# Kernel tuning notes

Hardware: AMD Instinct MI355X
Metric: run time of the kernel (lower is better)

## Reference

```python
import jax, jax.numpy as jnp
import numpy as np
from jax import lax

DN = ('NCHW', 'OIHW', 'NCHW')

def setup_inputs() -> dict:
    key = jax.random.key(0)
    ks = jax.random.split(key, 7)
    s = 0.05  # keep activations tame through 32 chained blocks
    return {
        'x':  jax.random.normal(ks[0], (16, 256, 64, 64), dtype=jnp.float32),
        'w1': jax.random.normal(ks[1], (32, 4, 256, 1, 1), dtype=jnp.float32) * s,
        'b1': jax.random.normal(ks[2], (32, 4), dtype=jnp.float32) * s,
        'w2': jax.random.normal(ks[3], (32, 4, 4, 3, 3), dtype=jnp.float32) * s,
        'b2': jax.random.normal(ks[4], (32, 4), dtype=jnp.float32) * s,
        'w3': jax.random.normal(ks[5], (32, 256, 4, 1, 1), dtype=jnp.float32) * s,
        'b3': jax.random.normal(ks[6], (32, 256), dtype=jnp.float32) * s,
    }

def _block(x, w1, c1, w2, c2, w3, c3):
    # 1x1 reduce -> relu -> 3x3 same -> relu -> 1x1 expand -> relu
    h = jax.nn.relu(lax.conv_general_dilated(x, w1, (1, 1), 'VALID', dimension_numbers=DN)
                    + c1[None, :, None, None])
    h = jax.nn.relu(lax.conv_general_dilated(h, w2, (1, 1), 'SAME', dimension_numbers=DN)
                    + c2[None, :, None, None])
    h = jax.nn.relu(lax.conv_general_dilated(h, w3, (1, 1), 'VALID', dimension_numbers=DN)
                    + c3[None, :, None, None])
    return h

def reference(x, w1, b1, w2, b2, w3, b3):
    def step(carry, ws):
        xc, acc = carry
        xc = _block(xc, *ws)
        return (xc, acc + xc), None
    init = (x, jnp.zeros_like(x))
    (_, acc), _ = lax.scan(step, init, (w1, b1, w2, b2, w3, b3))
    return acc  # sum of all 32 block outputs, [16,256,64,64]
```

## Files before the change

### kernel.cpp

```cpp
#include <hip/hip_runtime.h>


#define NN 16
#define HH 64
#define WW 64
#define CIN 256
#define CB 4
#define NBLK 32
#define PXT 32

__device__ __forceinline__ int pxs(int px) { return px ^ ((px >> 3) & 7); }

__global__ __launch_bounds__(256) void phaseA(
    const float* __restrict__ x, const float* __restrict__ w1,
    const float* __restrict__ b1, float* __restrict__ h1out) {
  __shared__ float4 w1s[CIN];
  __shared__ float4 part[4][WW];
  int tid = threadIdx.x;
  for (int i = tid; i < CIN * CB; i += 256) {
    int o = i >> 8, c = i & 255;
    ((float*)&w1s[c])[o] = w1[i];
  }
  __syncthreads();
  int y = blockIdx.x, n = blockIdx.y;
  int chunk = tid >> 6, px = tid & 63;
  int cbase = chunk * 64;
  const float* xp = x + ((n * CIN + cbase) * HH + y) * WW + px;
  float s0 = 0.f, s1 = 0.f, s2 = 0.f, s3 = 0.f;
#pragma unroll 8
  for (int i = 0; i < 64; ++i) {
    float xv = xp[i * HH * WW];
    float4 wv = w1s[cbase + i];
    s0 = fmaf(xv, wv.x, s0);
    s1 = fmaf(xv, wv.y, s1);
    s2 = fmaf(xv, wv.z, s2);
    s3 = fmaf(xv, wv.w, s3);
  }
  part[chunk][px] = make_float4(s0, s1, s2, s3);
  __syncthreads();
  int px2 = tid >> 2, o = tid & 3;
  float v = ((float*)&part[0][px2])[o] + ((float*)&part[1][px2])[o] +
            ((float*)&part[2][px2])[o] + ((float*)&part[3][px2])[o];
  v += b1[o];
  h1out[((n * HH + y) * WW + px2) * CB + o] = fmaxf(v, 0.f);
}

__global__ __launch_bounds__(256) void phaseB(
    const float* __restrict__ h1in, float* __restrict__ h1out,
    float* __restrict__ h2out,
    const float* __restrict__ w2, const float* __restrict__ b2,
    const float* __restrict__ w3, const float* __restrict__ b3,
    const float* __restrict__ w1n, const float* __restrict__ b1n,
    int compute_next) {
  __shared__ float4 wpk[CIN][2];
  __shared__ float4 b3p[64];
  __shared__ __align__(16) float uni[8192];
  float4* h2pv = (float4*)uni;
  float4* combv = (float4*)uni;
  float4 (*h1t)[18] = (float4(*)[18])uni;

  int tid = threadIdx.x;
  int tx = blockIdx.x, ty = blockIdx.y, n = blockIdx.z;
  int x0 = tx * 16, y0 = ty * 16;

  {
    int c = tid;
    wpk[c][0] = *(const float4*)&w3[c * 4];
    float4 wt;
    wt.x = w1n[c];
    wt.y = w1n[256 + c];
    wt.z = w1n[512 + c];
    wt.w = w1n[768 + c];
    wpk[c][1] = wt;
    if (tid < 64) b3p[tid] = *(const float4*)&b3[tid * 4];
  }
  for (int t = tid; t < 324; t += 256) {
    int cy = t / 18, cx = t % 18;
    int gy = y0 + cy - 1, gx = x0 + cx - 1;
    float4 v = make_float4(0.f, 0.f, 0.f, 0.f);
    if (gy >= 0 && gy < HH && gx >= 0 && gx < WW)
      v = *(const float4*)&h1in[((n * HH + gy) * WW + gx) * CB];
    h1t[cy][cx] = v;
  }
  __syncthreads();

  int lx = tid & 15, ly = tid >> 4;

  float4 hacc = make_float4(b2[0], b2[1], b2[2], b2[3]);
#pragma unroll
  for (int p = 0; p < 9; ++p) {
    int dy = p / 3, dx = p % 3;
    float4 hv = h1t[ly + dy][lx + dx];
#pragma unroll
    for (int i = 0; i < 4; ++i) {
      float hvi = (i == 0) ? hv.x : (i == 1) ? hv.y : (i == 2) ? hv.z : hv.w;
      hacc.x = fmaf(hvi, w2[(0 * 4 + i) * 9 + p], hacc.x);
      hacc.y = fmaf(hvi, w2[(1 * 4 + i) * 9 + p], hacc.y);
      hacc.z = fmaf(hvi, w2[(2 * 4 + i) * 9 + p], hacc.z);
      hacc.w = fmaf(hvi, w2[(3 * 4 + i) * 9 + p], hacc.w);
    }
  }
  float4 h2 = make_float4(fmaxf(hacc.x, 0.f), fmaxf(hacc.y, 0.f),
                          fmaxf(hacc.z, 0.f), fmaxf(hacc.w, 0.f));

  int gy = y0 + ly, gx = x0 + lx;
  int pxg = (n * HH + gy) * WW + gx;
  *(float4*)&h2out[pxg * CB] = h2;

  __syncthreads();
  h2pv[pxs(tid)] = h2;
  __syncthreads();

  int pg = tid & 31, q = tid >> 5;
  float4 h2r[8];
#pragma unroll
  for (int j = 0; j < 8; ++j) h2r[j] = h2pv[pxs(pg * 8 + j)];

  float4 tp[8];
#pragma unroll
  for (int j = 0; j < 8; ++j) tp[j] = make_float4(0.f, 0.f, 0.f, 0.f);

  int cbase = q * 32;
  for (int i4 = 0; i4 < 8; ++i4) {
    float4 bv = b3p[q * 8 + i4];
#pragma unroll
    for (int s = 0; s < 4; ++s) {
      int c = cbase + i4 * 4 + s;
      float b = (s == 0) ? bv.x : (s == 1) ? bv.y : (s == 2) ? bv.z : bv.w;
      float4 w3v = wpk[c][0];
      float4 wnv = wpk[c][1];
#pragma unroll
      for (int j = 0; j < 8; ++j) {
        float u = fmaf(h2r[j].x, w3v.x, b);
        u = fmaf(h2r[j].y, w3v.y, u);
        u = fmaf(h2r[j].z, w3v.z, u);
        u = fmaf(h2r[j].w, w3v.w, u);
        float v = fmaxf(u, 0.f);
        tp[j].x = fmaf(v, wnv.x, tp[j].x);
        tp[j].y = fmaf(v, wnv.y, tp[j].y);
        tp[j].z = fmaf(v, wnv.z, tp[j].z);
        tp[j].w = fmaf(v, wnv.w, tp[j].w);
      }
    }
  }

  __syncthreads();
#pragma unroll
  for (int j = 0; j < 8; ++j)
    combv[q * 256 + pxs(pg * 8 + j)] = tp[j];
  __syncthreads();

  if (compute_next) {
    float4 t = combv[0 * 256 + pxs(tid)];
#pragma unroll
    for (int qq = 1; qq < 8; ++qq) {
      float4 pv = combv[qq * 256 + pxs(tid)];
      t.x += pv.x; t.y += pv.y; t.z += pv.z; t.w += pv.w;
    }
    float4 r = make_float4(fmaxf(t.x + b1n[0], 0.f), fmaxf(t.y + b1n[1], 0.f),
                           fmaxf(t.z + b1n[2], 0.f), fmaxf(t.w + b1n[3], 0.f));
    *(float4*)&h1out[pxg * CB] = r;
  }
}

__global__ __launch_bounds__(256, 4) void phaseC(
    const float* __restrict__ h2buf, const float* __restrict__ w3g,
    const float* __restrict__ b3g, float* __restrict__ out) {
  __shared__ float4 h2s[2][PXT];
  __shared__ float tr[CIN][PXT + 1];
  int tid = threadIdx.x;
  int p0 = blockIdx.x * PXT;
  int n = blockIdx.y;
  float acc[PXT];
#pragma unroll
  for (int i = 0; i < PXT; ++i) acc[i] = 0.f;

  if (tid < PXT)
    h2s[0][tid] = *(const float4*)&h2buf[((0 * NN + n) * 4096 + p0 + tid) * 4];
  __syncthreads();

  for (int k = 0; k < NBLK; ++k) {
    float4 wv = *(const float4*)&w3g[(k * 256 + tid) * 4];
    float bv = b3g[k * 256 + tid];
    if (k + 1 < NBLK && tid < PXT)
      h2s[(k + 1) & 1][tid] =
          *(const float4*)&h2buf[(((k + 1) * NN + n) * 4096 + p0 + tid) * 4];
    const float4* hb = h2s[k & 1];
#pragma unroll
    for (int i = 0; i < PXT; ++i) {
      float4 h = hb[i];
      float u = fmaf(h.w, wv.w,
                fmaf(h.z, wv.z, fmaf(h.y, wv.y, fmaf(h.x, wv.x, bv))));
      acc[i] += fmaxf(u, 0.f);
    }
    __syncthreads();
  }

#pragma unroll
  for (int i = 0; i < PXT; ++i) tr[tid][i] = acc[i];
  __syncthreads();
  int xi = tid & 31, cb = tid >> 5;
#pragma unroll
  for (int j = 0; j < 32; ++j) {
    int c = cb + j * 8;
    out[(n * CIN + c) * (HH * WW) + p0 + xi] = tr[c][xi];
  }
}

extern "C" void kernel_launch(void* const* d_in, const int* in_sizes, int n_in,
                              void* d_out, int out_size, void* d_ws, size_t ws_size,
                              hipStream_t stream) {
  const float* x  = (const float*)d_in[0];
  const float* w1 = (const float*)d_in[1];
  const float* b1 = (const float*)d_in[2];
  const float* w2 = (const float*)d_in[3];
  const float* b2 = (const float*)d_in[4];
  const float* w3 = (const float*)d_in[5];
  const float* b3 = (const float*)d_in[6];
  float* out = (float*)d_out;
  float* ws = (float*)d_ws;

  const int STATE = NN * HH * WW * CB;
  float* h1a = ws;
  float* h1b = ws + STATE;
  float* h2  = ws + 2 * STATE;

  phaseA<<<dim3(HH, NN), 256, 0, stream>>>(x, w1, b1, h1a);
  for (int k = 0; k < NBLK; ++k) {
    const float* hin = (k & 1) ? h1b : h1a;
    float* hout = (k & 1) ? h1a : h1b;
    int kn = (k < NBLK - 1) ? k + 1 : NBLK - 1;
    phaseB<<<dim3(4, 4, NN), 256, 0, stream>>>(
        hin, hout, h2 + k * STATE,
        w2 + k * 144, b2 + k * CB, w3 + k * 1024, b3 + k * 256,
        w1 + kn * 1024, b1 + kn * CB, (k < NBLK - 1) ? 1 : 0);
  }
  phaseC<<<dim3((HH * WW) / PXT, NN), 256, 0, stream>>>(h2, w3, b3, out);
}
```

Before: 515.3 us.

## Halve phaseB tile height to double grid and split channels across 16 groups

phaseB now processes 16x8 pixel tiles instead of 16x16, launching 512 blocks per block-step instead of 256 so more of the GPU's compute units are occupied during the 32 serial launches. The 3x3 conv uses only half the threads, and the fused expand/next-reduce work is split into 16 channel groups of 16 instead of 8 groups of 32, with a 16-way reduction in shared memory. Launch bounds request 2 blocks per SM. In exchange there is more halo overhead, idle threads during the 3x3 stage and a larger shared-memory reduction.

```diff
diff --git a/kernel.cpp b/kernel.cpp
--- a/kernel.cpp
+++ b/kernel.cpp
@@ -45,7 +45,7 @@
   h1out[((n * HH + y) * WW + px2) * CB + o] = fmaxf(v, 0.f);
 }
 
-__global__ __launch_bounds__(256) void phaseB(
+__global__ __launch_bounds__(256, 2) void phaseB(
     const float* __restrict__ h1in, float* __restrict__ h1out,
     float* __restrict__ h2out,
     const float* __restrict__ w2, const float* __restrict__ b2,
@@ -54,14 +54,14 @@
     int compute_next) {
   __shared__ float4 wpk[CIN][2];
   __shared__ float4 b3p[64];
-  __shared__ __align__(16) float uni[8192];
-  float4* h2pv = (float4*)uni;
-  float4* combv = (float4*)uni;
+  __shared__ float4 h2sb[128];
+  __shared__ __align__(16) float4 uni[2048];
   float4 (*h1t)[18] = (float4(*)[18])uni;
+  float4* comb = (float4*)uni;
 
   int tid = threadIdx.x;
   int tx = blockIdx.x, ty = blockIdx.y, n = blockIdx.z;
-  int x0 = tx * 16, y0 = ty * 16;
+  int x0 = tx * 16, y0 = ty * 8;
 
   {
     int c = tid;
@@ -74,8 +74,8 @@
     wpk[c][1] = wt;
     if (tid < 64) b3p[tid] = *(const float4*)&b3[tid * 4];
   }
-  for (int t = tid; t < 324; t += 256) {
-    int cy = t / 18, cx = t % 18;
+  if (tid < 180) {
+    int cy = tid / 18, cx = tid % 18;
     int gy = y0 + cy - 1, gx = x0 + cx - 1;
     float4 v = make_float4(0.f, 0.f, 0.f, 0.f);
     if (gy >= 0 && gy < HH && gx >= 0 && gx < WW)
@@ -84,48 +84,46 @@
   }
   __syncthreads();
 
-  int lx = tid & 15, ly = tid >> 4;
-
-  float4 hacc = make_float4(b2[0], b2[1], b2[2], b2[3]);
-#pragma unroll
-  for (int p = 0; p < 9; ++p) {
-    int dy = p / 3, dx = p % 3;
-    float4 hv = h1t[ly + dy][lx + dx];
-#pragma unroll
-    for (int i = 0; i < 4; ++i) {
-      float hvi = (i == 0) ? hv.x : (i == 1) ? hv.y : (i == 2) ? hv.z : hv.w;
-      hacc.x = fmaf(hvi, w2[(0 * 4 + i) * 9 + p], hacc.x);
-      hacc.y = fmaf(hvi, w2[(1 * 4 + i) * 9 + p], hacc.y);
-      hacc.z = fmaf(hvi, w2[(2 * 4 + i) * 9 + p], hacc.z);
-      hacc.w = fmaf(hvi, w2[(3 * 4 + i) * 9 + p], hacc.w);
-    }
-  }
-  float4 h2 = make_float4(fmaxf(hacc.x, 0.f), fmaxf(hacc.y, 0.f),
-                          fmaxf(hacc.z, 0.f), fmaxf(hacc.w, 0.f));
-
-  int gy = y0 + ly, gx = x0 + lx;
-  int pxg = (n * HH + gy) * WW + gx;
-  *(float4*)&h2out[pxg * CB] = h2;
-
-  __syncthreads();
-  h2pv[pxs(tid)] = h2;
-  __syncthreads();
-
-  int pg = tid & 31, q = tid >> 5;
+  if (tid < 128) {
+    int lx = tid & 15, ly = tid >> 4;
+    float4 hacc = make_float4(b2[0], b2[1], b2[2], b2[3]);
+#pragma unroll
+    for (int p = 0; p < 9; ++p) {
+      int dy = p / 3, dx = p % 3;
+      float4 hv = h1t[ly + dy][lx + dx];
+#pragma unroll
+      for (int i = 0; i < 4; ++i) {
+        float hvi = (i == 0) ? hv.x : (i == 1) ? hv.y : (i == 2) ? hv.z : hv.w;
+        hacc.x = fmaf(hvi, w2[(0 * 4 + i) * 9 + p], hacc.x);
+        hacc.y = fmaf(hvi, w2[(1 * 4 + i) * 9 + p], hacc.y);
+        hacc.z = fmaf(hvi, w2[(2 * 4 + i) * 9 + p], hacc.z);
+        hacc.w = fmaf(hvi, w2[(3 * 4 + i) * 9 + p], hacc.w);
+      }
+    }
+    float4 h2 = make_float4(fmaxf(hacc.x, 0.f), fmaxf(hacc.y, 0.f),
+                            fmaxf(hacc.z, 0.f), fmaxf(hacc.w, 0.f));
+    int gy = y0 + ly, gx = x0 + lx;
+    int pxg = (n * HH + gy) * WW + gx;
+    *(float4*)&h2out[pxg * CB] = h2;
+    h2sb[pxs(tid)] = h2;
+  }
+  __syncthreads();
+
+  int pg = tid & 15, q = tid >> 4;
   float4 h2r[8];
 #pragma unroll
-  for (int j = 0; j < 8; ++j) h2r[j] = h2pv[pxs(pg * 8 + j)];
+  for (int j = 0; j < 8; ++j) h2r[j] = h2sb[pxs(pg * 8 + j)];
 
   float4 tp[8];
 #pragma unroll
   for (int j = 0; j < 8; ++j) tp[j] = make_float4(0.f, 0.f, 0.f, 0.f);
 
-  int cbase = q * 32;
-  for (int i4 = 0; i4 < 8; ++i4) {
-    float4 bv = b3p[q * 8 + i4];
+#pragma unroll
+  for (int i4 = 0; i4 < 4; ++i4) {
+    float4 bv = b3p[q * 4 + i4];
 #pragma unroll
     for (int s = 0; s < 4; ++s) {
-      int c = cbase + i4 * 4 + s;
+      int c = q * 16 + i4 * 4 + s;
       float b = (s == 0) ? bv.x : (s == 1) ? bv.y : (s == 2) ? bv.z : bv.w;
       float4 w3v = wpk[c][0];
       float4 wnv = wpk[c][1];
@@ -144,22 +142,23 @@
     }
   }
 
-  __syncthreads();
 #pragma unroll
   for (int j = 0; j < 8; ++j)
-    combv[q * 256 + pxs(pg * 8 + j)] = tp[j];
-  __syncthreads();
-
-  if (compute_next) {
-    float4 t = combv[0 * 256 + pxs(tid)];
-#pragma unroll
-    for (int qq = 1; qq < 8; ++qq) {
-      float4 pv = combv[qq * 256 + pxs(tid)];
+    comb[q * 128 + pxs(pg * 8 + j)] = tp[j];
+  __syncthreads();
+
+  if (compute_next && tid < 128) {
+    int p = tid;
+    float4 t = comb[pxs(p)];
+#pragma unroll
+    for (int qq = 1; qq < 16; ++qq) {
+      float4 pv = comb[qq * 128 + pxs(p)];
       t.x += pv.x; t.y += pv.y; t.z += pv.z; t.w += pv.w;
     }
     float4 r = make_float4(fmaxf(t.x + b1n[0], 0.f), fmaxf(t.y + b1n[1], 0.f),
                            fmaxf(t.z + b1n[2], 0.f), fmaxf(t.w + b1n[3], 0.f));
-    *(float4*)&h1out[pxg * CB] = r;
+    int gy = y0 + (p >> 4), gx = x0 + (p & 15);
+    *(float4*)&h1out[((n * HH + gy) * WW + gx) * CB] = r;
   }
 }
 
@@ -230,7 +229,7 @@
     const float* hin = (k & 1) ? h1b : h1a;
     float* hout = (k & 1) ? h1a : h1b;
     int kn = (k < NBLK - 1) ? k + 1 : NBLK - 1;
-    phaseB<<<dim3(4, 4, NN), 256, 0, stream>>>(
+    phaseB<<<dim3(4, 8, NN), 256, 0, stream>>>(
         hin, hout, h2 + k * STATE,
         w2 + k * 144, b2 + k * CB, w3 + k * 1024, b3 + k * 256,
         w1 + kn * 1024, b1 + kn * CB, (k < NBLK - 1) ? 1 : 0);
```

Result: faster. 463.8 us (-10.0%).
